# Kernel tuning notes

Hardware: AMD Instinct MI355X
Metric: run time of the kernel (lower is better)

## Reference

```python
import jax, jax.numpy as jnp
import numpy as np

B, N, D = 2, 2048, 1024
H, DH = 16, 64
FF = 4096


def _layernorm(x, g, b, eps=1e-5):
    mu = jnp.mean(x, axis=-1, keepdims=True)
    var = jnp.var(x, axis=-1, keepdims=True)
    return (x - mu) * jax.lax.rsqrt(var + eps) * g + b


def setup_inputs() -> dict:
    key = jax.random.key(0)
    ks = jax.random.split(key, 8)
    s = 0.02  # realistic init scale so softmax is well-behaved
    return {
        "x": jax.random.normal(ks[0], (B, N, D), jnp.float32),
        "wq": jax.random.normal(ks[1], (D, H * DH), jnp.float32) * s,
        "wk": jax.random.normal(ks[2], (D, H * DH), jnp.float32) * s,
        "wv": jax.random.normal(ks[3], (D, H * DH), jnp.float32) * s,
        "wo": jax.random.normal(ks[4], (H * DH, D), jnp.float32) * s,
        "w1": jax.random.normal(ks[5], (D, FF), jnp.float32) * s,
        "b1": jnp.zeros((FF,), jnp.float32),
        "w2": jax.random.normal(ks[6], (FF, D), jnp.float32) * s,
        "b2": jnp.zeros((D,), jnp.float32),
        "ln1_g": jnp.ones((D,), jnp.float32),
        "ln1_b": jnp.zeros((D,), jnp.float32),
        "ln2_g": jnp.ones((D,), jnp.float32),
        "ln2_b": jnp.zeros((D,), jnp.float32),
    }


def reference(x, wq, wk, wv, wo, w1, b1, w2, b2, ln1_g, ln1_b, ln2_g, ln2_b):
    # --- pre-norm self-attention (encoder path, no masks/mem/topk) ---
    res = x
    h = _layernorm(x, ln1_g, ln1_b)
    q = (h @ wq).reshape(B, N, H, DH).transpose(0, 2, 1, 3)  # b h n d
    k = (h @ wk).reshape(B, N, H, DH).transpose(0, 2, 1, 3)
    v = (h @ wv).reshape(B, N, H, DH).transpose(0, 2, 1, 3)
    # NOTE: source has NO 1/sqrt(d) scaling
    dots = jnp.einsum("bhid,bhjd->bhij", q, k)
    attn = jax.nn.softmax(dots.astype(jnp.float32), axis=-1).astype(dots.dtype)
    out = jnp.einsum("bhij,bhjd->bhid", attn, v)
    out = out.transpose(0, 2, 1, 3).reshape(B, N, H * DH) @ wo
    x = out + res
    # --- pre-norm feedforward (exact GELU) ---
    res = x
    h = _layernorm(x, ln2_g, ln2_b)
    h = jax.nn.gelu(h @ w1 + b1, approximate=False)
    x = (h @ w2 + b2) + res
    return x
```

## Files before the change

### kernel.cpp

```cpp
#include <hip/hip_runtime.h>
#include <math.h>
#include <stdint.h>

#define B_  2
#define N_  2048
#define D_  1024
#define H_  16
#define DH_ 64
#define FF_ 4096
#define M_  (B_ * N_)

typedef __bf16 bf16;
typedef float  f32x4  __attribute__((ext_vector_type(4)));
typedef __bf16 bf16x8 __attribute__((ext_vector_type(8)));
typedef __bf16 bf16x4 __attribute__((ext_vector_type(4)));

__device__ __forceinline__ void async_copy16(const void* g, void* l) {
    __builtin_amdgcn_global_load_lds((__attribute__((address_space(1))) unsigned int*)g,
                                     (__attribute__((address_space(3))) unsigned int*)l,
                                     16, 0, 0);
}

__global__ __launch_bounds__(256) void ln_kernel(const float* __restrict__ x,
                                                 const float* __restrict__ g,
                                                 const float* __restrict__ bta,
                                                 bf16* __restrict__ y)
{
    const int row = blockIdx.x;
    const int t = threadIdx.x;
    const float4 v = ((const float4*)(x + (size_t)row * D_))[t];
    float s  = v.x + v.y + v.z + v.w;
    float s2 = v.x * v.x + v.y * v.y + v.z * v.z + v.w * v.w;
#pragma unroll
    for (int o = 32; o > 0; o >>= 1) {
        s  += __shfl_down(s, o);
        s2 += __shfl_down(s2, o);
    }
    __shared__ float red[8];
    const int wid = t >> 6;
    if ((t & 63) == 0) { red[wid] = s; red[4 + wid] = s2; }
    __syncthreads();
    if (t == 0) {
        red[0] = red[0] + red[1] + red[2] + red[3];
        red[4] = red[4] + red[5] + red[6] + red[7];
    }
    __syncthreads();
    const float mean = red[0] * (1.0f / D_);
    const float var  = red[4] * (1.0f / D_) - mean * mean;
    const float rstd = rsqrtf(var + 1e-5f);
    const float4 gg = ((const float4*)g)[t];
    const float4 bb = ((const float4*)bta)[t];
    bf16x4 o;
    o[0] = (bf16)((v.x - mean) * rstd * gg.x + bb.x);
    o[1] = (bf16)((v.y - mean) * rstd * gg.y + bb.y);
    o[2] = (bf16)((v.z - mean) * rstd * gg.z + bb.z);
    o[3] = (bf16)((v.w - mean) * rstd * gg.w + bb.w);
    ((bf16x4*)(y + (size_t)row * D_))[t] = o;
}

__global__ __launch_bounds__(256) void transpose_bf16(const float* __restrict__ in,
                                                      bf16* __restrict__ out,
                                                      int R, int C)
{
    __shared__ float tile[32][33];
    const int c0 = blockIdx.x * 32, r0 = blockIdx.y * 32;
    const int tx = threadIdx.x, ty = threadIdx.y;
#pragma unroll
    for (int i = 0; i < 4; i++)
        tile[ty + i * 8][tx] = in[(size_t)(r0 + ty + i * 8) * C + c0 + tx];
    __syncthreads();
#pragma unroll
    for (int i = 0; i < 4; i++)
        out[(size_t)(c0 + ty + i * 8) * R + r0 + tx] = (bf16)tile[tx][ty + i * 8];
}

__global__ __launch_bounds__(256) void transpose3_bf16(const float* __restrict__ a,
                                                       const float* __restrict__ b,
                                                       const float* __restrict__ c,
                                                       bf16* __restrict__ out)
{
    __shared__ float tile[32][33];
    const float* in = (blockIdx.z == 0) ? a : (blockIdx.z == 1) ? b : c;
    bf16* o = out + (size_t)blockIdx.z * D_ * D_;
    const int c0 = blockIdx.x * 32, r0 = blockIdx.y * 32;
    const int tx = threadIdx.x, ty = threadIdx.y;
#pragma unroll
    for (int i = 0; i < 4; i++)
        tile[ty + i * 8][tx] = in[(size_t)(r0 + ty + i * 8) * D_ + c0 + tx];
    __syncthreads();
#pragma unroll
    for (int i = 0; i < 4; i++)
        o[(size_t)(c0 + ty + i * 8) * D_ + r0 + tx] = (bf16)tile[tx][ty + i * 8];
}

template <int EPI, int OMODE>
__global__ __launch_bounds__(256) void mfma_gemm(const bf16* __restrict__ A,
                                                 const bf16* __restrict__ Bt,
                                                 void* __restrict__ Cout,
                                                 int M, int N, int K,
                                                 const float* __restrict__ bias,
                                                 const float* __restrict__ res)
{
    __shared__ bf16 As[128 * 32];
    __shared__ bf16 Bs[128 * 32];
    const int t = threadIdx.x;
    const int w = t >> 6, lane = t & 63;
    const int wr = w >> 1, wc = w & 1;
    const int m0 = blockIdx.y * 128, n0 = blockIdx.x * 128;
    const int lr = lane & 15, lg = lane >> 4;
    const size_t MDc = (size_t)M_ * D_;

    f32x4 acc[4][4];
#pragma unroll
    for (int m = 0; m < 4; m++)
#pragma unroll
        for (int n = 0; n < 4; n++) acc[m][n] = {0.f, 0.f, 0.f, 0.f};

    const int q0c = w * 2, q1c = w * 2 + 1;
    const int row0 = q0c * 16 + (lane >> 2);
    const int row1 = q1c * 16 + (lane >> 2);
    const int kk = (lane & 3) * 8;

    for (int k0 = 0; k0 < K; k0 += 32) {
        async_copy16(A  + (size_t)(m0 + row0) * K + k0 + kk, &As[q0c * 512]);
        async_copy16(A  + (size_t)(m0 + row1) * K + k0 + kk, &As[q1c * 512]);
        async_copy16(Bt + (size_t)(n0 + row0) * K + k0 + kk, &Bs[q0c * 512]);
        async_copy16(Bt + (size_t)(n0 + row1) * K + k0 + kk, &Bs[q1c * 512]);
        __syncthreads();

        bf16x8 af[4], bfr[4];
#pragma unroll
        for (int m = 0; m < 4; m++)
            af[m] = *(const bf16x8*)&As[(wr * 64 + m * 16 + lr) * 32 + lg * 8];
#pragma unroll
        for (int n = 0; n < 4; n++)
            bfr[n] = *(const bf16x8*)&Bs[(wc * 64 + n * 16 + lr) * 32 + lg * 8];
#pragma unroll
        for (int m = 0; m < 4; m++)
#pragma unroll
            for (int n = 0; n < 4; n++)
                acc[m][n] = __builtin_amdgcn_mfma_f32_16x16x32_bf16(
                    af[m], bfr[n], acc[m][n], 0, 0, 0);
        __syncthreads();
    }

#pragma unroll
    for (int m = 0; m < 4; m++)
#pragma unroll
        for (int n = 0; n < 4; n++) {
            const int col = n0 + wc * 64 + n * 16 + lr;
            const float bv = (EPI >= 2) ? bias[col] : 0.f;
            if (OMODE == 3) {
                const int slice = col >> 10;
                const int c = col & 1023;
                if (slice == 2) {
                    const int head = c >> 6, dh = c & 63;
                    const int row0_ = m0 + wr * 64 + m * 16 + lg * 4;
                    const int bb = row0_ >> 11, nn = row0_ & 2047;
                    bf16x4 st;
#pragma unroll
                    for (int r2 = 0; r2 < 4; r2++) st[r2] = (bf16)acc[m][n][r2];
                    *(bf16x4*)((bf16*)Cout + 2 * MDc +
                               (size_t)((bb * H_ + head) * DH_ + dh) * N_ + nn) = st;
                } else {
                    bf16* dst = (bf16*)Cout + (size_t)slice * MDc;
#pragma unroll
                    for (int r2 = 0; r2 < 4; r2++) {
                        const int row = m0 + wr * 64 + m * 16 + lg * 4 + r2;
                        dst[(size_t)row * D_ + c] = (bf16)acc[m][n][r2];
                    }
                }
            } else {
#pragma unroll
                for (int r2 = 0; r2 < 4; r2++) {
                    const int row = m0 + wr * 64 + m * 16 + lg * 4 + r2;
                    float v = acc[m][n][r2] + bv;
                    if (EPI == 1 || EPI == 3) v += res[(size_t)row * N + col];
                    if (EPI == 2) v = 0.5f * v * (1.0f + erff(v * 0.70710678118654752f));
                    if (OMODE == 1) ((bf16*)Cout)[(size_t)row * N + col] = (bf16)v;
                    else            ((float*)Cout)[(size_t)row * N + col] = v;
                }
            }
        }
}

__global__ __launch_bounds__(256) void mfma_attn(const bf16* __restrict__ Q,
                                                 const bf16* __restrict__ K,
                                                 const bf16* __restrict__ Vt,
                                                 bf16* __restrict__ O)
{
    const int qt = blockIdx.x, h = blockIdx.y, b = blockIdx.z;
    const int t = threadIdx.x, w = t >> 6, lane = t & 63;
    const int lr = lane & 15, lg = lane >> 4;

    __shared__ bf16 Ks[2][64 * 64];
    __shared__ bf16 Vs[2][64 * 64];
    __shared__ bf16 Ps[4][32 * 72];

    const int q0 = qt * 128 + w * 32;
    bf16x8 a_q[2][2];
#pragma unroll
    for (int mi = 0; mi < 2; mi++)
#pragma unroll
        for (int ki = 0; ki < 2; ki++)
            a_q[mi][ki] = *(const bf16x8*)&Q[(size_t)(b * N_ + q0 + mi * 16 + lr) * (H_ * DH_)
                                            + h * DH_ + ki * 32 + lg * 8];

    f32x4 acc_o[2][4];
#pragma unroll
    for (int mi = 0; mi < 2; mi++)
#pragma unroll
        for (int nd = 0; nd < 4; nd++) acc_o[mi][nd] = {0.f, 0.f, 0.f, 0.f};
    float m_run[2][4], l_run[2][4];
#pragma unroll
    for (int mi = 0; mi < 2; mi++)
#pragma unroll
        for (int r2 = 0; r2 < 4; r2++) { m_run[mi][r2] = -3.0e38f; l_run[mi][r2] = 0.f; }

    const int srow = lane >> 3;
    const int schunk = (lane & 7) ^ srow;
    const size_t kbase = (size_t)b * N_ * (H_ * DH_) + (size_t)h * DH_ + schunk * 8;
    const size_t vbase = ((size_t)(b * H_ + h) * DH_) * N_;

    auto stage = [&](int kv0, int buf) {
#pragma unroll
        for (int i = 0; i < 2; i++) {
            const int r = w * 16 + i * 8 + srow;
            async_copy16(&K[kbase + (size_t)(kv0 + r) * (H_ * DH_)],
                         &Ks[buf][(w * 16 + i * 8) * 64]);
            async_copy16(&Vt[vbase + (size_t)r * N_ + kv0 + schunk * 8],
                         &Vs[buf][(w * 16 + i * 8) * 64]);
        }
    };

    stage(0, 0);
    const int NT = N_ / 64;
    for (int it = 0; it < NT; ++it) {
        __syncthreads();
        if (it + 1 < NT) stage((it + 1) * 64, (it + 1) & 1);
        const bf16* ks = Ks[it & 1];
        const bf16* vs = Vs[it & 1];

        f32x4 s[2][4];
#pragma unroll
        for (int mi = 0; mi < 2; mi++)
#pragma unroll
            for (int ni = 0; ni < 4; ni++) s[mi][ni] = {0.f, 0.f, 0.f, 0.f};
        __builtin_amdgcn_s_setprio(1);
#pragma unroll
        for (int ki = 0; ki < 2; ki++) {
            bf16x8 bk[4];
#pragma unroll
            for (int ni = 0; ni < 4; ni++) {
                const int r = ni * 16 + lr;
                const int slot = (lg + ki * 4) ^ (r & 7);
                bk[ni] = *(const bf16x8*)&ks[r * 64 + slot * 8];
            }
#pragma unroll
            for (int mi = 0; mi < 2; mi++)
#pragma unroll
                for (int ni = 0; ni < 4; ni++)
                    s[mi][ni] = __builtin_amdgcn_mfma_f32_16x16x32_bf16(
                        a_q[mi][ki], bk[ni], s[mi][ni], 0, 0, 0);
        }
        __builtin_amdgcn_s_setprio(0);

#pragma unroll
        for (int mi = 0; mi < 2; mi++) {
            float resc[4], rsum[4];
#pragma unroll
            for (int r2 = 0; r2 < 4; r2++) {
                float v0 = fmaxf(fmaxf(s[mi][0][r2], s[mi][1][r2]),
                                 fmaxf(s[mi][2][r2], s[mi][3][r2]));
#pragma unroll
                for (int off = 1; off <= 8; off <<= 1)
                    v0 = fmaxf(v0, __shfl_xor(v0, off));
                const float mn = fmaxf(m_run[mi][r2], v0);
                resc[r2] = __expf(m_run[mi][r2] - mn);
                m_run[mi][r2] = mn;
                rsum[r2] = 0.f;
            }
#pragma unroll
            for (int ni = 0; ni < 4; ni++)
#pragma unroll
                for (int r2 = 0; r2 < 4; r2++) {
                    const float p = __expf(s[mi][ni][r2] - m_run[mi][r2]);
                    rsum[r2] += p;
                    Ps[w][(mi * 16 + lg * 4 + r2) * 72 + ni * 16 + lr] = (bf16)p;
                }
#pragma unroll
            for (int r2 = 0; r2 < 4; r2++) {
                float sr = rsum[r2];
#pragma unroll
                for (int off = 1; off <= 8; off <<= 1) sr += __shfl_xor(sr, off);
                l_run[mi][r2] = l_run[mi][r2] * resc[r2] + sr;
#pragma unroll
                for (int nd = 0; nd < 4; nd++) acc_o[mi][nd][r2] *= resc[r2];
            }
        }

        bf16x8 a_p[2][2];
#pragma unroll
        for (int mi = 0; mi < 2; mi++)
#pragma unroll
            for (int k2 = 0; k2 < 2; k2++)
                a_p[mi][k2] = *(const bf16x8*)&Ps[w][(mi * 16 + lr) * 72 + k2 * 32 + lg * 8];
        __builtin_amdgcn_s_setprio(1);
#pragma unroll
        for (int k2 = 0; k2 < 2; k2++) {
            bf16x8 bv[4];
#pragma unroll
            for (int nd = 0; nd < 4; nd++) {
                const int r = nd * 16 + lr;
                const int slot = (lg + k2 * 4) ^ (r & 7);
                bv[nd] = *(const bf16x8*)&vs[r * 64 + slot * 8];
            }
#pragma unroll
            for (int mi = 0; mi < 2; mi++)
#pragma unroll
                for (int nd = 0; nd < 4; nd++)
                    acc_o[mi][nd] = __builtin_amdgcn_mfma_f32_16x16x32_bf16(
                        a_p[mi][k2], bv[nd], acc_o[mi][nd], 0, 0, 0);
        }
        __builtin_amdgcn_s_setprio(0);
    }

#pragma unroll
    for (int mi = 0; mi < 2; mi++) {
        float inv[4];
#pragma unroll
        for (int r2 = 0; r2 < 4; r2++) inv[r2] = 1.f / l_run[mi][r2];
#pragma unroll
        for (int nd = 0; nd < 4; nd++)
#pragma unroll
            for (int r2 = 0; r2 < 4; r2++) {
                const int qrow = q0 + mi * 16 + lg * 4 + r2;
                const int d = nd * 16 + lr;
                O[(size_t)(b * N_ + qrow) * (H_ * DH_) + h * DH_ + d] =
                    (bf16)(acc_o[mi][nd][r2] * inv[r2]);
            }
    }
}

extern "C" void kernel_launch(void* const* d_in, const int* in_sizes, int n_in,
                              void* d_out, int out_size, void* d_ws, size_t ws_size,
                              hipStream_t stream)
{
    const float* x     = (const float*)d_in[0];
    const float* wq    = (const float*)d_in[1];
    const float* wk    = (const float*)d_in[2];
    const float* wv    = (const float*)d_in[3];
    const float* wo    = (const float*)d_in[4];
    const float* w1    = (const float*)d_in[5];
    const float* b1    = (const float*)d_in[6];
    const float* w2    = (const float*)d_in[7];
    const float* b2    = (const float*)d_in[8];
    const float* ln1_g = (const float*)d_in[9];
    const float* ln1_b = (const float*)d_in[10];
    const float* ln2_g = (const float*)d_in[11];
    const float* ln2_b = (const float*)d_in[12];

    const size_t MD = (size_t)M_ * D_;
    char* wsb = (char*)d_ws;
    auto alloc = [&](size_t bytes) { char* p = wsb; wsb += (bytes + 255) & ~(size_t)255; return p; };
    bf16*  hb    = (bf16*)alloc(MD * 2);
    bf16*  qb    = (bf16*)alloc(MD * 2 * 3);
    bf16*  kb    = qb + MD;
    bf16*  vtb   = qb + 2 * MD;
    bf16*  ab    = (bf16*)alloc(MD * 2);
    float* x1    = (float*)alloc(MD * 4);
    bf16*  h2b   = (bf16*)alloc(MD * 2);
    bf16*  ffb   = (bf16*)alloc((size_t)M_ * FF_ * 2);
    bf16*  wqkvT = (bf16*)alloc((size_t)3 * D_ * D_ * 2);
    bf16*  woT   = (bf16*)alloc((size_t)D_ * D_ * 2);
    bf16*  w1T   = (bf16*)alloc((size_t)D_ * FF_ * 2);
    bf16*  w2T   = (bf16*)alloc((size_t)FF_ * D_ * 2);

    dim3 tb(32, 8);
    transpose3_bf16<<<dim3(D_ / 32, D_ / 32, 3), tb, 0, stream>>>(wq, wk, wv, wqkvT);
    transpose_bf16<<<dim3(D_ / 32, D_ / 32), tb, 0, stream>>>(wo, woT, D_, D_);
    transpose_bf16<<<dim3(FF_ / 32, D_ / 32), tb, 0, stream>>>(w1, w1T, D_, FF_);
    transpose_bf16<<<dim3(D_ / 32, FF_ / 32), tb, 0, stream>>>(w2, w2T, FF_, D_);

    ln_kernel<<<M_, 256, 0, stream>>>(x, ln1_g, ln1_b, hb);

    mfma_gemm<0, 3><<<dim3(3 * D_ / 128, M_ / 128), 256, 0, stream>>>(
        hb, wqkvT, qb, M_, 3 * D_, D_, nullptr, nullptr);

    mfma_attn<<<dim3(N_ / 128, H_, B_), 256, 0, stream>>>(qb, kb, vtb, ab);

    dim3 gP(D_ / 128, M_ / 128);
    mfma_gemm<1, 0><<<gP, 256, 0, stream>>>(ab, woT, x1, M_, D_, D_, nullptr, x);

    ln_kernel<<<M_, 256, 0, stream>>>(x1, ln2_g, ln2_b, h2b);

    mfma_gemm<2, 1><<<dim3(FF_ / 128, M_ / 128), 256, 0, stream>>>(
        h2b, w1T, ffb, M_, FF_, D_, b1, nullptr);

    mfma_gemm<3, 0><<<dim3(D_ / 128, M_ / 128), 256, 0, stream>>>(
        ffb, w2T, (float*)d_out, M_, D_, FF_, b2, x1);
}
```

Measured before the change: 476.3 us.

## Restructure attention to 8 waves of 16 query rows with transposed MFMA operands

The attention kernel now launches 512 threads per block, and each of the 8 waves handles 16 query rows instead of 32. S and O are computed transposed (K/V as the A operand, Q/P as B), so each lane holds a whole query column. That turns the row max and row sum into two cross-lane shuffles, lets the output be written as vectorized bf16x4 stores, and lets P be written to LDS as bf16x2. It also halves per-wave register use, which raises occupancy (launch bounds 512,4) to hide latency. The trade-off is that each K/V fragment read from LDS now feeds only one MFMA instead of two.

```diff
diff --git a/kernel.cpp b/kernel.cpp
--- a/kernel.cpp
+++ b/kernel.cpp
@@ -14,6 +14,7 @@
 typedef float  f32x4  __attribute__((ext_vector_type(4)));
 typedef __bf16 bf16x8 __attribute__((ext_vector_type(8)));
 typedef __bf16 bf16x4 __attribute__((ext_vector_type(4)));
+typedef __bf16 bf16x2 __attribute__((ext_vector_type(2)));
 
 __device__ __forceinline__ void async_copy16(const void* g, void* l) {
     __builtin_amdgcn_global_load_lds((__attribute__((address_space(1))) unsigned int*)g,
@@ -184,10 +185,10 @@
         }
 }
 
-__global__ __launch_bounds__(256) void mfma_attn(const bf16* __restrict__ Q,
-                                                 const bf16* __restrict__ K,
-                                                 const bf16* __restrict__ Vt,
-                                                 bf16* __restrict__ O)
+__global__ __launch_bounds__(512, 4) void mfma_attn(const bf16* __restrict__ Q,
+                                                    const bf16* __restrict__ K,
+                                                    const bf16* __restrict__ Vt,
+                                                    bf16* __restrict__ O)
 {
     const int qt = blockIdx.x, h = blockIdx.y, b = blockIdx.z;
     const int t = threadIdx.x, w = t >> 6, lane = t & 63;
@@ -195,42 +196,29 @@
 
     __shared__ bf16 Ks[2][64 * 64];
     __shared__ bf16 Vs[2][64 * 64];
-    __shared__ bf16 Ps[4][32 * 72];
-
-    const int q0 = qt * 128 + w * 32;
-    bf16x8 a_q[2][2];
-#pragma unroll
-    for (int mi = 0; mi < 2; mi++)
-#pragma unroll
-        for (int ki = 0; ki < 2; ki++)
-            a_q[mi][ki] = *(const bf16x8*)&Q[(size_t)(b * N_ + q0 + mi * 16 + lr) * (H_ * DH_)
-                                            + h * DH_ + ki * 32 + lg * 8];
-
-    f32x4 acc_o[2][4];
-#pragma unroll
-    for (int mi = 0; mi < 2; mi++)
-#pragma unroll
-        for (int nd = 0; nd < 4; nd++) acc_o[mi][nd] = {0.f, 0.f, 0.f, 0.f};
-    float m_run[2][4], l_run[2][4];
-#pragma unroll
-    for (int mi = 0; mi < 2; mi++)
-#pragma unroll
-        for (int r2 = 0; r2 < 4; r2++) { m_run[mi][r2] = -3.0e38f; l_run[mi][r2] = 0.f; }
+    __shared__ bf16 Ps[8][16 * 72];
+
+    const int q0w = qt * 128 + w * 16;
+    bf16x8 b_q[2];
+#pragma unroll
+    for (int ki = 0; ki < 2; ki++)
+        b_q[ki] = *(const bf16x8*)&Q[(size_t)(b * N_ + q0w + lr) * (H_ * DH_)
+                                     + h * DH_ + ki * 32 + lg * 8];
+
+    f32x4 acc[4];
+#pragma unroll
+    for (int nd = 0; nd < 4; nd++) acc[nd] = {0.f, 0.f, 0.f, 0.f};
+    float m_run = -3.0e38f, l_run = 0.f;
 
     const int srow = lane >> 3;
     const int schunk = (lane & 7) ^ srow;
-    const size_t kbase = (size_t)b * N_ * (H_ * DH_) + (size_t)h * DH_ + schunk * 8;
-    const size_t vbase = ((size_t)(b * H_ + h) * DH_) * N_;
+    const int r_st = w * 8 + srow;
 
     auto stage = [&](int kv0, int buf) {
-#pragma unroll
-        for (int i = 0; i < 2; i++) {
-            const int r = w * 16 + i * 8 + srow;
-            async_copy16(&K[kbase + (size_t)(kv0 + r) * (H_ * DH_)],
-                         &Ks[buf][(w * 16 + i * 8) * 64]);
-            async_copy16(&Vt[vbase + (size_t)r * N_ + kv0 + schunk * 8],
-                         &Vs[buf][(w * 16 + i * 8) * 64]);
-        }
+        async_copy16(&K[(size_t)(b * N_ + kv0 + r_st) * (H_ * DH_) + h * DH_ + schunk * 8],
+                     &Ks[buf][w * 8 * 64]);
+        async_copy16(&Vt[((size_t)(b * H_ + h) * DH_ + r_st) * N_ + kv0 + schunk * 8],
+                     &Vs[buf][w * 8 * 64]);
     };
 
     stage(0, 0);
@@ -241,104 +229,85 @@
         const bf16* ks = Ks[it & 1];
         const bf16* vs = Vs[it & 1];
 
-        f32x4 s[2][4];
-#pragma unroll
-        for (int mi = 0; mi < 2; mi++)
-#pragma unroll
-            for (int ni = 0; ni < 4; ni++) s[mi][ni] = {0.f, 0.f, 0.f, 0.f};
+        f32x4 s[4];
+#pragma unroll
+        for (int ni = 0; ni < 4; ni++) s[ni] = {0.f, 0.f, 0.f, 0.f};
         __builtin_amdgcn_s_setprio(1);
 #pragma unroll
-        for (int ki = 0; ki < 2; ki++) {
-            bf16x8 bk[4];
+        for (int ki = 0; ki < 2; ki++)
 #pragma unroll
             for (int ni = 0; ni < 4; ni++) {
                 const int r = ni * 16 + lr;
                 const int slot = (lg + ki * 4) ^ (r & 7);
-                bk[ni] = *(const bf16x8*)&ks[r * 64 + slot * 8];
-            }
-#pragma unroll
-            for (int mi = 0; mi < 2; mi++)
-#pragma unroll
-                for (int ni = 0; ni < 4; ni++)
-                    s[mi][ni] = __builtin_amdgcn_mfma_f32_16x16x32_bf16(
-                        a_q[mi][ki], bk[ni], s[mi][ni], 0, 0, 0);
-        }
+                const bf16x8 bk = *(const bf16x8*)&ks[r * 64 + slot * 8];
+                s[ni] = __builtin_amdgcn_mfma_f32_16x16x32_bf16(
+                    bk, b_q[ki], s[ni], 0, 0, 0);
+            }
         __builtin_amdgcn_s_setprio(0);
 
-#pragma unroll
-        for (int mi = 0; mi < 2; mi++) {
-            float resc[4], rsum[4];
+        float pmax = s[0][0];
+#pragma unroll
+        for (int ni = 0; ni < 4; ni++)
+#pragma unroll
+            for (int r2 = 0; r2 < 4; r2++)
+                pmax = fmaxf(pmax, s[ni][r2]);
+        pmax = fmaxf(pmax, __shfl_xor(pmax, 16));
+        pmax = fmaxf(pmax, __shfl_xor(pmax, 32));
+        const float mn = fmaxf(m_run, pmax);
+        const float resc = __expf(m_run - mn);
+        m_run = mn;
+
+        float p[4][4];
+        float rsum = 0.f;
+#pragma unroll
+        for (int ni = 0; ni < 4; ni++)
 #pragma unroll
             for (int r2 = 0; r2 < 4; r2++) {
-                float v0 = fmaxf(fmaxf(s[mi][0][r2], s[mi][1][r2]),
-                                 fmaxf(s[mi][2][r2], s[mi][3][r2]));
-#pragma unroll
-                for (int off = 1; off <= 8; off <<= 1)
-                    v0 = fmaxf(v0, __shfl_xor(v0, off));
-                const float mn = fmaxf(m_run[mi][r2], v0);
-                resc[r2] = __expf(m_run[mi][r2] - mn);
-                m_run[mi][r2] = mn;
-                rsum[r2] = 0.f;
-            }
-#pragma unroll
-            for (int ni = 0; ni < 4; ni++)
-#pragma unroll
-                for (int r2 = 0; r2 < 4; r2++) {
-                    const float p = __expf(s[mi][ni][r2] - m_run[mi][r2]);
-                    rsum[r2] += p;
-                    Ps[w][(mi * 16 + lg * 4 + r2) * 72 + ni * 16 + lr] = (bf16)p;
-                }
-#pragma unroll
-            for (int r2 = 0; r2 < 4; r2++) {
-                float sr = rsum[r2];
-#pragma unroll
-                for (int off = 1; off <= 8; off <<= 1) sr += __shfl_xor(sr, off);
-                l_run[mi][r2] = l_run[mi][r2] * resc[r2] + sr;
-#pragma unroll
-                for (int nd = 0; nd < 4; nd++) acc_o[mi][nd][r2] *= resc[r2];
-            }
-        }
-
-        bf16x8 a_p[2][2];
-#pragma unroll
-        for (int mi = 0; mi < 2; mi++)
-#pragma unroll
-            for (int k2 = 0; k2 < 2; k2++)
-                a_p[mi][k2] = *(const bf16x8*)&Ps[w][(mi * 16 + lr) * 72 + k2 * 32 + lg * 8];
+                p[ni][r2] = __expf(s[ni][r2] - mn);
+                rsum += p[ni][r2];
+            }
+        rsum += __shfl_xor(rsum, 16);
+        rsum += __shfl_xor(rsum, 32);
+        l_run = l_run * resc + rsum;
+#pragma unroll
+        for (int nd = 0; nd < 4; nd++)
+#pragma unroll
+            for (int r2 = 0; r2 < 4; r2++) acc[nd][r2] *= resc;
+
+#pragma unroll
+        for (int ni = 0; ni < 4; ni++)
+#pragma unroll
+            for (int hh = 0; hh < 2; hh++) {
+                bf16x2 pr;
+                pr[0] = (bf16)p[ni][2 * hh + 0];
+                pr[1] = (bf16)p[ni][2 * hh + 1];
+                *(bf16x2*)&Ps[w][lr * 72 + ni * 16 + lg * 4 + hh * 2] = pr;
+            }
+
         __builtin_amdgcn_s_setprio(1);
 #pragma unroll
         for (int k2 = 0; k2 < 2; k2++) {
-            bf16x8 bv[4];
+            const bf16x8 bp = *(const bf16x8*)&Ps[w][lr * 72 + k2 * 32 + lg * 8];
 #pragma unroll
             for (int nd = 0; nd < 4; nd++) {
                 const int r = nd * 16 + lr;
                 const int slot = (lg + k2 * 4) ^ (r & 7);
-                bv[nd] = *(const bf16x8*)&vs[r * 64 + slot * 8];
-            }
-#pragma unroll
-            for (int mi = 0; mi < 2; mi++)
-#pragma unroll
-                for (int nd = 0; nd < 4; nd++)
-                    acc_o[mi][nd] = __builtin_amdgcn_mfma_f32_16x16x32_bf16(
-                        a_p[mi][k2], bv[nd], acc_o[mi][nd], 0, 0, 0);
+                const bf16x8 av = *(const bf16x8*)&vs[r * 64 + slot * 8];
+                acc[nd] = __builtin_amdgcn_mfma_f32_16x16x32_bf16(
+                    av, bp, acc[nd], 0, 0, 0);
+            }
         }
         __builtin_amdgcn_s_setprio(0);
     }
 
-#pragma unroll
-    for (int mi = 0; mi < 2; mi++) {
-        float inv[4];
-#pragma unroll
-        for (int r2 = 0; r2 < 4; r2++) inv[r2] = 1.f / l_run[mi][r2];
-#pragma unroll
-        for (int nd = 0; nd < 4; nd++)
-#pragma unroll
-            for (int r2 = 0; r2 < 4; r2++) {
-                const int qrow = q0 + mi * 16 + lg * 4 + r2;
-                const int d = nd * 16 + lr;
-                O[(size_t)(b * N_ + qrow) * (H_ * DH_) + h * DH_ + d] =
-                    (bf16)(acc_o[mi][nd][r2] * inv[r2]);
-            }
+    const float inv = 1.f / l_run;
+    const size_t obase = (size_t)(b * N_ + q0w + lr) * (H_ * DH_) + h * DH_;
+#pragma unroll
+    for (int nd = 0; nd < 4; nd++) {
+        bf16x4 o4;
+#pragma unroll
+        for (int r2 = 0; r2 < 4; r2++) o4[r2] = (bf16)(acc[nd][r2] * inv);
+        *(bf16x4*)&O[obase + nd * 16 + lg * 4] = o4;
     }
 }
 
@@ -387,7 +356,7 @@
     mfma_gemm<0, 3><<<dim3(3 * D_ / 128, M_ / 128), 256, 0, stream>>>(
         hb, wqkvT, qb, M_, 3 * D_, D_, nullptr, nullptr);
 
-    mfma_attn<<<dim3(N_ / 128, H_, B_), 256, 0, stream>>>(qb, kb, vtb, ab);
+    mfma_attn<<<dim3(N_ / 128, H_, B_), 512, 0, stream>>>(qb, kb, vtb, ab);
 
     dim3 gP(D_ / 128, M_ / 128);
     mfma_gemm<1, 0><<<gP, 256, 0, stream>>>(ab, woT, x1, M_, D_, D_, nullptr, x);
```

New measurement: 420.7 us. 1.13x faster.
